# Kernel optimization log

Hardware: AMD Instinct MI355X
Metric: run time of the kernel (lower is better)

The kernel has to match this reference:

```python
import jax, jax.numpy as jnp
import numpy as np

N_QUBITS = 5
N_A = 1
N_LAYERS = 4
PATCH = 2 ** (N_QUBITS - N_A)  # 16

CNOT4 = jnp.array([[1, 0, 0, 0], [0, 1, 0, 0], [0, 0, 0, 1], [0, 0, 1, 0]], dtype=jnp.complex64)


def _ry(t):
    c = jnp.cos(t / 2).astype(jnp.complex64)
    s = jnp.sin(t / 2).astype(jnp.complex64)
    return jnp.stack([jnp.stack([c, -s]), jnp.stack([s, c])])


def _rot(phi, theta, omega):
    # PennyLane Rot = RZ(omega) RY(theta) RZ(phi)
    c = jnp.cos(theta / 2)
    s = jnp.sin(theta / 2)
    ep = jnp.exp(-0.5j * (phi + omega))  # e^{-i(phi+omega)/2}
    em = jnp.exp(-0.5j * (phi - omega))  # e^{-i(phi-omega)/2}
    return jnp.stack([jnp.stack([ep * c, -jnp.conj(em) * s]),
                      jnp.stack([em * s, jnp.conj(ep) * c])])


def _apply_1q(state, U, w):
    # contract U onto qubit axis w of state [2]*5
    s = jnp.tensordot(U, state, axes=(1, w))
    return jnp.moveaxis(s, 0, w)


def _apply_cnot(state, c, t):
    perm = jnp.moveaxis(state, (c, t), (0, 1))
    shp = perm.shape
    out = (CNOT4 @ perm.reshape(4, -1)).reshape(shp)
    return jnp.moveaxis(out, (0, 1), (c, t))


def _simulate(noise, w):
    # noise: [5], w: [4,5,3] -> normalized probs over first 16 basis states
    state = jnp.zeros((2,) * N_QUBITS, jnp.complex64).at[(0,) * N_QUBITS].set(1.0)
    for q in range(N_QUBITS):
        state = _apply_1q(state, _ry(noise[q]), q)
    for l in range(N_LAYERS):
        r = l % (N_QUBITS - 1) + 1  # StronglyEntanglingLayers default ranges
        for q in range(N_QUBITS):
            state = _apply_1q(state, _rot(w[l, q, 0], w[l, q, 1], w[l, q, 2]), q)
        for q in range(N_QUBITS):
            state = _apply_cnot(state, q, (q + r) % N_QUBITS)
    probs = jnp.abs(state.reshape(-1)) ** 2  # [32]
    p0 = probs[:PATCH] / jnp.sum(probs)  # partial measure: ancilla wire 4 == 0
    return p0 / jnp.max(p0)


def setup_inputs() -> dict:
    key = jax.random.key(0)
    k1, k2 = jax.random.split(key)
    B, G = 65536, 4
    x = jax.random.uniform(k1, (B, N_QUBITS), dtype=jnp.float32)
    weights = jax.random.uniform(k2, (G, N_LAYERS, N_QUBITS, 3), dtype=jnp.float32)  # q_delta=1
    return {"x": x, "weights": weights}


def reference(x, weights):
    sim_g = jax.vmap(_simulate, in_axes=(None, 0))   # over generators
    sim_bg = jax.vmap(sim_g, in_axes=(0, None))      # over batch
    out = sim_bg(x, weights)                         # [B, G, 16]
    return out.reshape(x.shape[0], -1).astype(jnp.float32)  # [B, G*16]
```

## Files before the change

### kernel.cpp

```cpp
#include <hip/hip_runtime.h>


#define NGEN 4
#define NLAY 4
#define NQ   5

typedef _Float16 half8 __attribute__((ext_vector_type(8)));
typedef float    f32x4 __attribute__((ext_vector_type(4)));

#define WAVE_SYNC()                                                  \
    do {                                                             \
        __builtin_amdgcn_wave_barrier();                             \
        asm volatile("s_waitcnt lgkmcnt(0)" ::: "memory");           \
        __builtin_amdgcn_wave_barrier();                             \
    } while (0)

__global__ __launch_bounds__(256) void pqg_fused(
    const float* __restrict__ x,
    const float* __restrict__ wts,
    float* __restrict__ out)
{
    __shared__ float  gm[NGEN][NLAY * NQ * 8];
    __shared__ float2 cs[NGEN][16 * 33];
    __shared__ float  scS[NGEN][640];
    __shared__ float  scC[NGEN][640];

    const int t    = threadIdx.x;
    const int lane = t & 63;
    const int g    = t >> 6;
    const int b0   = blockIdx.x * 128;
    const int cg   = lane >> 4;
    const int m    = lane & 15;

    if (lane < NLAY * NQ) {
        const float* wp = wts + (g * (NLAY * NQ) + lane) * 3;
        const float phi = wp[0], theta = wp[1], omega = wp[2];
        const float a = 0.5f * (phi + omega);
        const float bb = 0.5f * (phi - omega);
        const float h = 0.5f * theta;
        const float sa = __sinf(a), ca = __cosf(a);
        const float sb = __sinf(bb), cb = __cosf(bb);
        const float st = __sinf(h), ct = __cosf(h);
        float* mm = &gm[g][lane * 8];
        mm[0] =  ca * ct;  mm[1] = -sa * ct;
        mm[2] = -cb * st;  mm[3] = -sb * st;
        mm[4] =  cb * st;  mm[5] = -sb * st;
        mm[6] =  ca * ct;  mm[7] =  sa * ct;
    }

#pragma unroll
    for (int e = 0; e < 10; ++e) {
        const int idx = e * 64 + lane;
        const float tt = 0.5f * x[(size_t)b0 * 5 + idx];
        scS[g][idx] = __sinf(tt);
        scC[g][idx] = __cosf(tt);
    }
    WAVE_SYNC();

    float mr[8], mi[8];
#pragma unroll
    for (int j = 0; j < 8; ++j) {
        mr[j] = (cg * 8 + j == m) ? 1.0f : 0.0f;
        mi[j] = 0.0f;
    }

#pragma unroll
    for (int l = NLAY - 1; l >= 0; --l) {
#pragma unroll
        for (int j = 0; j < 8; ++j)
            cs[g][m * 33 + cg * 8 + j] = make_float2(mr[j], mi[j]);
        WAVE_SYNC();
        {
            float2 tmp[8];
#pragma unroll
            for (int j = 0; j < 8; ++j) {
                int v = cg * 8 + j;
#pragma unroll
                for (int q = 0; q < NQ; ++q) {
                    const int cb = 16 >> q;
                    int tq = q + l + 1; if (tq >= NQ) tq -= NQ;
                    const int tb = 16 >> tq;
                    if (v & cb) v ^= tb;
                }
                tmp[j] = cs[g][m * 33 + v];
            }
            WAVE_SYNC();
#pragma unroll
            for (int j = 0; j < 8; ++j) { mr[j] = tmp[j].x; mi[j] = tmp[j].y; }
        }

#pragma unroll
        for (int q = NQ - 1; q >= 2; --q) {
            const float4 u0 = *(const float4*)&gm[g][(l * NQ + q) * 8];
            const float4 u1 = *(const float4*)&gm[g][(l * NQ + q) * 8 + 4];
            const float u00r = u0.x, u00i = u0.y, u01r = u0.z, u01i = u0.w;
            const float u10r = u1.x, u10i = u1.y, u11r = u1.z, u11i = u1.w;
            const int sb = 16 >> q;
#pragma unroll
            for (int ja = 0; ja < 8; ++ja) {
                if (!(ja & sb)) {
                    const int jb = ja | sb;
                    const float ar = mr[ja], ai = mi[ja];
                    const float br = mr[jb], bi = mi[jb];
                    mr[ja] = u00r * ar - u00i * ai + u10r * br - u10i * bi;
                    mi[ja] = u00r * ai + u00i * ar + u10r * bi + u10i * br;
                    mr[jb] = u01r * ar - u01i * ai + u11r * br - u11i * bi;
                    mi[jb] = u01r * ai + u01i * ar + u11r * bi + u11i * br;
                }
            }
        }

#pragma unroll
        for (int q = 1; q >= 0; --q) {
            const float4 u0 = *(const float4*)&gm[g][(l * NQ + q) * 8];
            const float4 u1 = *(const float4*)&gm[g][(l * NQ + q) * 8 + 4];
            const float u00r = u0.x, u00i = u0.y, u01r = u0.z, u01i = u0.w;
            const float u10r = u1.x, u10i = u1.y, u11r = u1.z, u11i = u1.w;
            const int sb = 16 >> q;
#pragma unroll
            for (int j = 0; j < 8; ++j)
                cs[g][m * 33 + cg * 8 + j] = make_float2(mr[j], mi[j]);
            WAVE_SYNC();
            const int ibase = (cg * 8) & ~sb;
            const int jbase = (cg * 8) |  sb;
            const bool hi = ((cg * 8) & sb) != 0;
            const float k0r = hi ? u01r : u00r, k0i = hi ? u01i : u00i;
            const float k1r = hi ? u11r : u10r, k1i = hi ? u11i : u10i;
#pragma unroll
            for (int j = 0; j < 8; ++j) {
                const float2 A2 = cs[g][m * 33 + ibase + j];
                const float2 B2 = cs[g][m * 33 + jbase + j];
                mr[j] = k0r * A2.x - k0i * A2.y + k1r * B2.x - k1i * B2.y;
                mi[j] = k0r * A2.y + k0i * A2.x + k1r * B2.y + k1i * B2.x;
            }
            WAVE_SYNC();
        }
    }

    half8 Ar, Ai;
#pragma unroll
    for (int j = 0; j < 8; ++j) {
        Ar[j] = (_Float16)mr[j];
        Ai[j] = (_Float16)mi[j];
    }

    const int quad = cg;
    const int n    = m;

#pragma unroll
    for (int t8 = 0; t8 < 8; ++t8) {
        const int bl = t8 * 16 + n;
        const int b  = b0 + bl;
        const float* C = &scC[g][bl * 5];
        const float* S = &scS[g][bl * 5];

        const float f01 = ((quad & 2) ? S[0] : C[0]) * ((quad & 1) ? S[1] : C[1]);
        const float a0 = f01 * C[2], a1 = f01 * S[2];
        const float b00 = a0 * C[3], b01 = a0 * S[3];
        const float b10 = a1 * C[3], b11 = a1 * S[3];

        half8 Bf;
        Bf[0] = (_Float16)(b00 * C[4]);  Bf[1] = (_Float16)(b00 * S[4]);
        Bf[2] = (_Float16)(b01 * C[4]);  Bf[3] = (_Float16)(b01 * S[4]);
        Bf[4] = (_Float16)(b10 * C[4]);  Bf[5] = (_Float16)(b10 * S[4]);
        Bf[6] = (_Float16)(b11 * C[4]);  Bf[7] = (_Float16)(b11 * S[4]);

        f32x4 accR = {0.f, 0.f, 0.f, 0.f};
        f32x4 accI = {0.f, 0.f, 0.f, 0.f};
        accR = __builtin_amdgcn_mfma_f32_16x16x32_f16(Ar, Bf, accR, 0, 0, 0);
        accI = __builtin_amdgcn_mfma_f32_16x16x32_f16(Ai, Bf, accI, 0, 0, 0);

        const float p0 = accR[0] * accR[0] + accI[0] * accI[0];
        const float p1 = accR[1] * accR[1] + accI[1] * accI[1];
        const float p2 = accR[2] * accR[2] + accI[2] * accI[2];
        const float p3 = accR[3] * accR[3] + accI[3] * accI[3];

        float mx = fmaxf(fmaxf(p0, p1), fmaxf(p2, p3));
        mx = fmaxf(mx, __shfl_xor(mx, 16));
        mx = fmaxf(mx, __shfl_xor(mx, 32));
        const float inv = 1.0f / mx;

        const float4 o = make_float4(p0 * inv, p1 * inv, p2 * inv, p3 * inv);
        *(float4*)(out + (size_t)b * 64 + g * 16 + quad * 4) = o;
    }
}

extern "C" void kernel_launch(void* const* d_in, const int* in_sizes, int n_in,
                              void* d_out, int out_size, void* d_ws, size_t ws_size,
                              hipStream_t stream) {
    const float* x = (const float*)d_in[0];
    const float* w = (const float*)d_in[1];
    float* out = (float*)d_out;
    const int B = in_sizes[0] / NQ;

    pqg_fused<<<B / 128, 256, 0, stream>>>(x, w, out);
}
```

Before: 68.98 us.

## Fuse CNOT permutation and two cross-lane qubit gates into one LDS exchange

The CNOT-ring permutation is folded into the read indices of the next layer's cross-lane gate stage, and the initial identity is pre-permuted. The two separate LDS round-trips for qubits 1 and 0 become a single exchange that applies their Kronecker-product 4x4 operator. This removes two LDS store/load/sync rounds per layer, at the cost of four LDS reads per element, extra FLOPs for building and applying the combined matrix, and a larger register footprint.

```diff
diff --git a/kernel.cpp b/kernel.cpp
--- a/kernel.cpp
+++ b/kernel.cpp
@@ -14,6 +14,17 @@
         asm volatile("s_waitcnt lgkmcnt(0)" ::: "memory");           \
         __builtin_amdgcn_wave_barrier();                             \
     } while (0)
+
+__device__ __forceinline__ int sigma5(int v, int l) {
+#pragma unroll
+    for (int q = 0; q < NQ; ++q) {
+        const int cb = 16 >> q;
+        int tq = q + l + 1; if (tq >= NQ) tq -= NQ;
+        const int tb = 16 >> tq;
+        if (v & cb) v ^= tb;
+    }
+    return v;
+}
 
 __global__ __launch_bounds__(256) void pqg_fused(
     const float* __restrict__ x,
@@ -60,35 +71,12 @@
     float mr[8], mi[8];
 #pragma unroll
     for (int j = 0; j < 8; ++j) {
-        mr[j] = (cg * 8 + j == m) ? 1.0f : 0.0f;
+        mr[j] = (sigma5(cg * 8 + j, NLAY - 1) == m) ? 1.0f : 0.0f;
         mi[j] = 0.0f;
     }
 
 #pragma unroll
     for (int l = NLAY - 1; l >= 0; --l) {
-#pragma unroll
-        for (int j = 0; j < 8; ++j)
-            cs[g][m * 33 + cg * 8 + j] = make_float2(mr[j], mi[j]);
-        WAVE_SYNC();
-        {
-            float2 tmp[8];
-#pragma unroll
-            for (int j = 0; j < 8; ++j) {
-                int v = cg * 8 + j;
-#pragma unroll
-                for (int q = 0; q < NQ; ++q) {
-                    const int cb = 16 >> q;
-                    int tq = q + l + 1; if (tq >= NQ) tq -= NQ;
-                    const int tb = 16 >> tq;
-                    if (v & cb) v ^= tb;
-                }
-                tmp[j] = cs[g][m * 33 + v];
-            }
-            WAVE_SYNC();
-#pragma unroll
-            for (int j = 0; j < 8; ++j) { mr[j] = tmp[j].x; mi[j] = tmp[j].y; }
-        }
-
 #pragma unroll
         for (int q = NQ - 1; q >= 2; --q) {
             const float4 u0 = *(const float4*)&gm[g][(l * NQ + q) * 8];
@@ -110,28 +98,58 @@
             }
         }
 
-#pragma unroll
-        for (int q = 1; q >= 0; --q) {
-            const float4 u0 = *(const float4*)&gm[g][(l * NQ + q) * 8];
-            const float4 u1 = *(const float4*)&gm[g][(l * NQ + q) * 8 + 4];
-            const float u00r = u0.x, u00i = u0.y, u01r = u0.z, u01i = u0.w;
-            const float u10r = u1.x, u10i = u1.y, u11r = u1.z, u11i = u1.w;
-            const int sb = 16 >> q;
+        {
+            const float4 q1a = *(const float4*)&gm[g][(l * NQ + 1) * 8];
+            const float4 q1b = *(const float4*)&gm[g][(l * NQ + 1) * 8 + 4];
+            const float4 q0a = *(const float4*)&gm[g][(l * NQ + 0) * 8];
+            const float4 q0b = *(const float4*)&gm[g][(l * NQ + 0) * 8 + 4];
+            const float a1r[2] = {q1a.x, q1a.z}, a1i[2] = {q1a.y, q1a.w};
+            const float b1r[2] = {q1b.x, q1b.z}, b1i[2] = {q1b.y, q1b.w};
+            const float a0r[2] = {q0a.x, q0a.z}, a0i[2] = {q0a.y, q0a.w};
+            const float b0r[2] = {q0b.x, q0b.z}, b0i[2] = {q0b.y, q0b.w};
+
+            float Kr[2][2][4], Ki[2][2][4];
+#pragma unroll
+            for (int b4 = 0; b4 < 2; ++b4) {
+#pragma unroll
+                for (int b3 = 0; b3 < 2; ++b3) {
+                    Kr[b4][b3][0] = a0r[b4] * a1r[b3] - a0i[b4] * a1i[b3];
+                    Ki[b4][b3][0] = a0r[b4] * a1i[b3] + a0i[b4] * a1r[b3];
+                    Kr[b4][b3][1] = a0r[b4] * b1r[b3] - a0i[b4] * b1i[b3];
+                    Ki[b4][b3][1] = a0r[b4] * b1i[b3] + a0i[b4] * b1r[b3];
+                    Kr[b4][b3][2] = b0r[b4] * a1r[b3] - b0i[b4] * a1i[b3];
+                    Ki[b4][b3][2] = b0r[b4] * a1i[b3] + b0i[b4] * a1r[b3];
+                    Kr[b4][b3][3] = b0r[b4] * b1r[b3] - b0i[b4] * b1i[b3];
+                    Ki[b4][b3][3] = b0r[b4] * b1i[b3] + b0i[b4] * b1r[b3];
+                }
+            }
+
 #pragma unroll
             for (int j = 0; j < 8; ++j)
                 cs[g][m * 33 + cg * 8 + j] = make_float2(mr[j], mi[j]);
             WAVE_SYNC();
-            const int ibase = (cg * 8) & ~sb;
-            const int jbase = (cg * 8) |  sb;
-            const bool hi = ((cg * 8) & sb) != 0;
-            const float k0r = hi ? u01r : u00r, k0i = hi ? u01i : u00i;
-            const float k1r = hi ? u11r : u10r, k1i = hi ? u11i : u10i;
+
 #pragma unroll
             for (int j = 0; j < 8; ++j) {
-                const float2 A2 = cs[g][m * 33 + ibase + j];
-                const float2 B2 = cs[g][m * 33 + jbase + j];
-                mr[j] = k0r * A2.x - k0i * A2.y + k1r * B2.x - k1i * B2.y;
-                mi[j] = k0r * A2.y + k0i * A2.x + k1r * B2.y + k1i * B2.x;
+                const int c = cg * 8 + j;
+                const int d = (l > 0) ? sigma5(c, l - 1) : c;
+                const int b4 = (d >> 4) & 1;
+                const int b3 = (d >> 3) & 1;
+                const int low = d & 7;
+                const float2 s0  = cs[g][m * 33 + low];
+                const float2 s8  = cs[g][m * 33 + low + 8];
+                const float2 s16 = cs[g][m * 33 + low + 16];
+                const float2 s24 = cs[g][m * 33 + low + 24];
+                float nr, ni;
+                nr  = Kr[b4][b3][0] * s0.x  - Ki[b4][b3][0] * s0.y;
+                ni  = Kr[b4][b3][0] * s0.y  + Ki[b4][b3][0] * s0.x;
+                nr += Kr[b4][b3][1] * s8.x  - Ki[b4][b3][1] * s8.y;
+                ni += Kr[b4][b3][1] * s8.y  + Ki[b4][b3][1] * s8.x;
+                nr += Kr[b4][b3][2] * s16.x - Ki[b4][b3][2] * s16.y;
+                ni += Kr[b4][b3][2] * s16.y + Ki[b4][b3][2] * s16.x;
+                nr += Kr[b4][b3][3] * s24.x - Ki[b4][b3][3] * s24.y;
+                ni += Kr[b4][b3][3] * s24.y + Ki[b4][b3][3] * s24.x;
+                mr[j] = nr; mi[j] = ni;
             }
             WAVE_SYNC();
         }
```

Measured after the change: 83.33 us. 1.21x slower.
